# Performance work log

Measured on AMD Instinct MI355X. Metric: run time of the kernel, lower is better.

## Reference

```python
import jax, jax.numpy as jnp
import numpy as np

TWO_PI = 2.0 * np.pi
ALPHA = 0.65
KSIZE = (3, 3, 3)   # (kOr, kH, kW)
ITERS = 1
BN_EPS = 1e-5


def _interp(v, dy, dx):
    """Bilinear sample of v[b,c,o, y+dy[o], x+dx[o]], border-clamped.
    v: [B,C,Or,H,W]; dy, dx: [Or] float per-orientation constant shifts."""
    H, W = v.shape[3], v.shape[4]
    y0 = jnp.floor(dy); fy = dy - y0; y0 = y0.astype(jnp.int32)
    iy = jnp.arange(H)[None, :] + y0[:, None]                      # [Or,H]
    g0 = jnp.take_along_axis(v, jnp.clip(iy, 0, H - 1)[None, None, :, :, None], axis=3)
    g1 = jnp.take_along_axis(v, jnp.clip(iy + 1, 0, H - 1)[None, None, :, :, None], axis=3)
    fyb = fy[None, None, :, None, None]
    v = (1.0 - fyb) * g0 + fyb * g1
    x0 = jnp.floor(dx); fx = dx - x0; x0 = x0.astype(jnp.int32)
    ix = jnp.arange(W)[None, :] + x0[:, None]                      # [Or,W]
    h0 = jnp.take_along_axis(v, jnp.clip(ix, 0, W - 1)[None, None, :, None, :], axis=4)
    h1 = jnp.take_along_axis(v, jnp.clip(ix + 1, 0, W - 1)[None, None, :, None, :], axis=4)
    fxb = fx[None, None, :, None, None]
    return (1.0 - fxb) * h0 + fxb * h1


def _convection(u, g0):
    """out[b,c,p] = u[b,c, p . g0[c]^{-1}] via trilinear resampling.
    Sample point: ((x,y) - R(theta - th0)@(x0,y0), theta - th0), theta periodic."""
    Or = u.shape[2]
    def one(uc, g):  # uc: [B,Or,H,W], g = (x0, y0, th0)
        x0, y0, th0 = g[0], g[1], g[2]
        t = th0 * Or / TWO_PI
        i = jnp.floor(t); f = t - i; i = i.astype(jnp.int32)
        # periodic linear interpolation along orientation axis
        v = (1.0 - f) * jnp.roll(uc, i, axis=1) + f * jnp.roll(uc, i + 1, axis=1)
        a = jnp.arange(Or, dtype=u.dtype) * (TWO_PI / Or) - th0
        dx = -(jnp.cos(a) * x0 - jnp.sin(a) * y0)
        dy = -(jnp.sin(a) * x0 + jnp.cos(a) * y0)
        return _interp(v[:, None], dy, dx)[:, 0]
    return jax.vmap(one, in_axes=(1, 0), out_axes=1)(u, g0)


def _se2_log(qx, qy, dth):
    """Exact SE(2) logarithm coordinates (c1,c2,c3) of group offset (qx,qy,dth)."""
    if abs(dth) < 1e-9:
        return qx, qy, dth
    h = 0.5 * dth
    cot = np.cos(h) / np.sin(h)
    return h * (qx * cot + qy), h * (-qx + qy * cot), dth


def _morph(u, metric, dilate):
    """Fractional morphological dilation (max of u(p.q) - k(q)) or erosion
    (min of u(p.q) + k(q)) with left-invariant Riemannian kernel
    k_c(q) = nu_a * d_c(q)^{2a/(2a-1)}, d_c^2 = (m0*c1)^2+(m1*c2)^2+(m2*c3)^2."""
    kOr, kH, kW = KSIZE
    Or = u.shape[2]
    thetas = jnp.arange(Or, dtype=u.dtype) * (TWO_PI / Or)
    p = 2.0 * ALPHA / (2.0 * ALPHA - 1.0)
    nu = (2.0 * ALPHA - 1.0) * (2.0 * ALPHA) ** (-p)
    out = None
    for qt in range(-(kOr // 2), kOr // 2 + 1):
        dth = qt * TWO_PI / Or
        for qy in range(-(kH // 2), kH // 2 + 1):
            for qx in range(-(kW // 2), kW // 2 + 1):
                c1, c2, c3 = _se2_log(float(qx), float(qy), dth)
                s = (metric[:, 0] * c1) ** 2 + (metric[:, 1] * c2) ** 2 + (metric[:, 2] * c3) ** 2
                k = nu * s ** (p / 2.0)                       # [C]
                # left-invariant shift: spatial offset rotated by theta_o
                dxo = jnp.cos(thetas) * qx - jnp.sin(thetas) * qy
                dyo = jnp.sin(thetas) * qx + jnp.cos(thetas) * qy
                val = _interp(jnp.roll(u, -qt, axis=2), dyo, dxo)
                kb = k[None, :, None, None, None]
                cand = val - kb if dilate else val + kb
                if out is None:
                    out = cand
                else:
                    out = jnp.maximum(out, cand) if dilate else jnp.minimum(out, cand)
    return out


def setup_inputs() -> dict:
    key = jax.random.key(0)
    ks = jax.random.split(key, 5)
    B, Cin, Cout, Or, H, W = 4, 8, 16, 8, 128, 128
    x = jax.random.normal(ks[0], (B, Cin, Or, H, W), dtype=jnp.float32)
    g0 = 0.5 * jax.random.normal(ks[1], (Cin, 3), dtype=jnp.float32)
    lo, hi = 1.4 / 3.0, 0.7 * 3.0   # reset_parameters range for metric params
    metric_dil = jax.random.uniform(ks[2], (Cin, 3), minval=lo, maxval=hi, dtype=jnp.float32)
    metric_ero = jax.random.uniform(ks[3], (Cin, 3), minval=lo, maxval=hi, dtype=jnp.float32)
    bound = 0.25  # kaiming_uniform(a=sqrt(5)) bound for [8,16] weight
    weight = jax.random.uniform(ks[4], (Cin, Cout), minval=-bound, maxval=bound, dtype=jnp.float32)
    gamma = jnp.ones((Cout,), jnp.float32)
    beta = jnp.zeros((Cout,), jnp.float32)
    return dict(x=x, g0=g0, metric_dil=metric_dil, metric_ero=metric_ero,
                weight=weight, gamma=gamma, beta=beta)


def reference(x, g0, metric_dil, metric_ero, weight, gamma, beta):
    u = x
    for _ in range(ITERS):
        u = _convection(u, g0)
        u = _morph(u, metric_dil, dilate=True)
        u = _morph(u, metric_ero, dilate=False)
    # channel mixing: [B,Cin,Or,H,W] x [Cin,Cout] -> [B,Cout,Or,H,W]
    y = jnp.einsum('bcohw,cd->bdohw', u, weight)
    # BatchNorm3d (training mode): per-channel stats over (B,Or,H,W)
    m = y.mean(axis=(0, 2, 3, 4), keepdims=True)
    v = y.var(axis=(0, 2, 3, 4), keepdims=True)
    yh = (y - m) * jax.lax.rsqrt(v + BN_EPS)
    return yh * gamma[None, :, None, None, None] + beta[None, :, None, None, None]
```

## Files before the change

### kernel.cpp

```cpp
#include <hip/hip_runtime.h>
#include <math.h>
#include <utility>

#define B 4
#define CIN 8
#define COUT 16
#define OR_ 8
#define H_ 128
#define W_ 128
#define HW 16384
#define PLANE HW
#define CH_STR (OR_*HW)
#define BATCH_STR (CIN*CH_STR)
#define NELEM (B*BATCH_STR)
#define NPOS (B*OR_*HW)
#define NB_RED 256

#define TILE 16
#define CB_DIM 24
#define CB_S   29
#define CB_PL  (CB_DIM*CB_S)
#define DB_DIM 20
#define DB_S   21
#define DB_PL  (DB_DIM*DB_S)

typedef __attribute__((ext_vector_type(4))) float f4;

struct Tables {
  float kdil[CIN][27];
  float kero[CIN][27];
  int   o1[CIN][OR_], o2[CIN][OR_];
  int   iy0[CIN][OR_], ix0[CIN][OR_];
  float w00[CIN][OR_], w01[CIN][OR_], w10[CIN][OR_], w11[CIN][OR_];
  float cf[CIN];
  int   iymin[CIN], iymax[CIN], ixmin[CIN], ixmax[CIN];
};

__host__ __device__ constexpr double m_cos(int o) {
  const double r = 0.70710678118654752440;
  const double t[8] = {1.0, r, 0.0, -r, -1.0, -r, 0.0, r};
  return t[o];
}
__host__ __device__ constexpr double m_sin(int o) {
  const double r = 0.70710678118654752440;
  const double t[8] = {0.0, r, 1.0, r, 0.0, -r, -1.0, -r};
  return t[o];
}
__host__ __device__ constexpr double tap_dx(int o, int j) {
  return m_cos(o)*(j % 3 - 1) - m_sin(o)*(j / 3 - 1);
}
__host__ __device__ constexpr double tap_dy(int o, int j) {
  return m_sin(o)*(j % 3 - 1) + m_cos(o)*(j / 3 - 1);
}
__host__ __device__ constexpr int ifloor(double v) {
  int i = (int)v;
  return ((double)i > v) ? i - 1 : i;
}
__host__ __device__ constexpr int tap_ix(int o, int j) { return ifloor(tap_dx(o, j)); }
__host__ __device__ constexpr int tap_iy(int o, int j) { return ifloor(tap_dy(o, j)); }
__host__ __device__ constexpr float tap_fx(int o, int j) { return (float)(tap_dx(o, j) - tap_ix(o, j)); }
__host__ __device__ constexpr float tap_fy(int o, int j) { return (float)(tap_dy(o, j) - tap_iy(o, j)); }
__host__ __device__ constexpr float corner_w(int o, int j, int dyb, int dxb) {
  float fy = tap_fy(o, j), fx = tap_fx(o, j);
  return (dyb ? fy : 1.0f - fy) * (dxb ? fx : 1.0f - fx);
}
__host__ __device__ constexpr int corner_r(int o, int j, int dyb) { return tap_iy(o, j) + dyb + 2; }
__host__ __device__ constexpr int corner_c(int o, int j, int i, int dxb) { return i + tap_ix(o, j) + dxb + 2; }
__host__ __device__ constexpr bool row_used(int o, int r) {
  for (int j = 0; j < 9; ++j)
    for (int dyb = 0; dyb < 2; ++dyb)
      for (int dxb = 0; dxb < 2; ++dxb)
        if (corner_w(o, j, dyb, dxb) != 0.0f && corner_r(o, j, dyb) == r)
          return true;
  return false;
}

template<int N> struct Rep {
  template<class F> __device__ __forceinline__ static void run(F&& f) {
    Rep<N-1>::run(f);
    f(std::integral_constant<int, N-1>{});
  }
};
template<> struct Rep<0> {
  template<class F> __device__ __forceinline__ static void run(F&&) {}
};


__global__ void precompute_kernel(const float* __restrict__ g0,
                                  const float* __restrict__ mdil,
                                  const float* __restrict__ mero,
                                  Tables* __restrict__ T) {
  const int t = threadIdx.x;
  const double TWO_PI = 6.283185307179586476925286766559;
  const double P  = 2.0*0.65/(2.0*0.65 - 1.0);
  const double NU = (2.0*0.65 - 1.0)*pow(2.0*0.65, -P);
  if (t < 432) {
    int which = t / 216;
    int r = t % 216;
    int c = r / 27;
    int j = r % 27;
    int qt = j/9 - 1;
    int qy = (j/3)%3 - 1;
    int qx = j%3 - 1;
    double dth = qt * (TWO_PI/OR_);
    double c1, c2, c3;
    if (qt == 0) { c1 = qx; c2 = qy; c3 = 0.0; }
    else {
      double h = 0.5*dth;
      double cot = cos(h)/sin(h);
      c1 = h*(qx*cot + qy);
      c2 = h*(-qx + qy*cot);
      c3 = dth;
    }
    const float* m = which ? mero : mdil;
    double a0 = (double)m[c*3+0]*c1;
    double a1 = (double)m[c*3+1]*c2;
    double a2 = (double)m[c*3+2]*c3;
    double s = a0*a0 + a1*a1 + a2*a2;
    float k = (float)(NU * pow(s, P*0.5));
    if (which) T->kero[c][j] = k; else T->kdil[c][j] = k;
  } else if (t >= 512 && t < 512 + CIN*OR_) {
    int r = t - 512;
    int c = r >> 3;
    int o = r & 7;
    float x0 = g0[c*3+0], y0 = g0[c*3+1], th0 = g0[c*3+2];
    float a = (float)(o*(TWO_PI/OR_)) - th0;
    float ca = cosf(a), sa = sinf(a);
    float dxv = -(ca*x0 - sa*y0);
    float dyv = -(sa*x0 + ca*y0);
    float fy0 = floorf(dyv), fx0 = floorf(dxv);
    float fy = dyv - fy0, fx = dxv - fx0;
    T->iy0[c][o] = (int)fy0;
    T->ix0[c][o] = (int)fx0;
    T->w00[c][o] = (1.f-fy)*(1.f-fx);
    T->w01[c][o] = (1.f-fy)*fx;
    T->w10[c][o] = fy*(1.f-fx);
    T->w11[c][o] = fy*fx;
    float tt = th0 * (float)(OR_/TWO_PI);
    float fi = floorf(tt);
    int ci = (int)fi;
    T->o1[c][o] = (o - ci) & 7;
    T->o2[c][o] = (o - ci - 1) & 7;
    if (o == 0) T->cf[c] = tt - fi;
  }
  __syncthreads();
  if (t < CIN) {
    int iymn = 999, iymx = -999, ixmn = 999, ixmx = -999;
    for (int o = 0; o < OR_; ++o) {
      iymn = min(iymn, T->iy0[t][o]); iymx = max(iymx, T->iy0[t][o]);
      ixmn = min(ixmn, T->ix0[t][o]); ixmx = max(ixmx, T->ix0[t][o]);
    }
    T->iymin[t] = iymn; T->iymax[t] = iymx;
    T->ixmin[t] = ixmn; T->ixmax[t] = ixmx;
  }
}

template<int O, int DIL, int PLSTR, int RSTR>
__device__ __forceinline__ void morph_tile_lds(const float* __restrict__ src,
                                               const float* __restrict__ kt,
                                               int row, int gc, float acc[4]) {
  Rep<3>::run([&](auto qc) {
    constexpr int qti = decltype(qc)::value;
    const float* p = src + ((O + qti + 7) & 7) * PLSTR + row * RSTR + gc;
    float win[5][8];
    Rep<5>::run([&](auto rc) {
      constexpr int r = decltype(rc)::value;
      if constexpr (row_used(O, r)) {
        #pragma unroll
        for (int k = 0; k < 8; ++k) win[r][k] = p[r*RSTR + k];
      }
    });
    Rep<9>::run([&](auto jc) {
      constexpr int j = decltype(jc)::value;
      float k = kt[qti*9 + j];
      float base = DIL ? -k : k;
      Rep<4>::run([&](auto ic) {
        constexpr int i = decltype(ic)::value;
        float v = base;
        Rep<4>::run([&](auto cc2) {
          constexpr int cn  = decltype(cc2)::value;
          constexpr int dyb = cn >> 1, dxb = cn & 1;
          constexpr float Wgt = corner_w(O, j, dyb, dxb);
          if constexpr (Wgt != 0.0f) {
            constexpr int R = corner_r(O, j, dyb);
            constexpr int C = corner_c(O, j, i, dxb);
            v = fmaf(Wgt, win[R][C], v);
          }
        });
        acc[i] = DIL ? fmaxf(acc[i], v) : fminf(acc[i], v);
      });
    });
  });
}

template<int O>
__device__ __forceinline__ void dil_wave(const float* __restrict__ cb, float* __restrict__ db,
                                         const float* __restrict__ kt, int lane) {
  #pragma unroll
  for (int it = 0; it < 2; ++it) {
    int g = lane + it*64;
    if (g < 100) {
      int row = g / 5;
      int gc = (g - row*5) * 4;
      float acc[4] = {-INFINITY, -INFINITY, -INFINITY, -INFINITY};
      morph_tile_lds<O, 1, CB_PL, CB_S>(cb, kt, row, gc, acc);
      float* d = db + O*DB_PL + row*DB_S + gc;
      #pragma unroll
      for (int i = 0; i < 4; ++i) d[i] = acc[i];
    }
  }
}

template<int O>
__device__ __forceinline__ void ero_wave(const float* __restrict__ db, float* __restrict__ dst,
                                         const float* __restrict__ kt, int lane) {
  int row = lane >> 2;
  int gc = (lane & 3) * 4;
  float acc[4] = {INFINITY, INFINITY, INFINITY, INFINITY};
  morph_tile_lds<O, 0, DB_PL, DB_S>(db, kt, row, gc, acc);
  f4 v = {acc[0], acc[1], acc[2], acc[3]};
  *(f4*)(dst + O*PLANE + row*W_ + gc) = v;
}

__global__ __launch_bounds__(512, 4)
void fused_kernel(const float* __restrict__ x, float* __restrict__ u3,
                  const Tables* __restrict__ T) {
  __shared__ float convbuf[8*CB_PL];
  __shared__ float dilbuf[8*DB_PL];
  int blk = blockIdx.x;
  int tx = blk & 7, ty = (blk >> 3) & 7, c = (blk >> 6) & 7, b = blk >> 9;
  int h0 = ty*TILE, w0 = tx*TILE;
  int t = threadIdx.x;
  int wid = t >> 6, lane = t & 63;
  const float* xc = x + b*BATCH_STR + c*CH_STR;

  {
    const int o = wid;
    const int iy0 = T->iy0[c][o], ix0 = T->ix0[c][o];
    const float w00 = T->w00[c][o], w01 = T->w01[c][o];
    const float w10 = T->w10[c][o], w11 = T->w11[c][o];
    const float cfv = T->cf[c];
    const float* p1 = xc + T->o1[c][o]*PLANE;
    const float* p2 = xc + T->o2[c][o]*PLANE;
    bool interior = (h0 - 4 + T->iymin[c] >= 0) & (h0 + 20 + T->iymax[c] <= 127)
                  & (w0 - 4 + T->ixmin[c] >= 0) & (w0 + 20 + T->ixmax[c] <= 127)
                  & (h0 >= 16) & (h0 <= 96) & (w0 >= 16) & (w0 <= 96);
    if (interior) {
      #pragma unroll
      for (int it = 0; it < 3; ++it) {
        int q = lane + it*64;
        if (q < 144) {
          int r = q / 6;
          int cq = q - r*6;
          int iy = h0 - 4 + r + iy0;
          int ix = w0 - 4 + cq*4 + ix0;
          const float* q1 = p1 + iy*W_ + ix;
          const float* q2 = p2 + iy*W_ + ix;
          float a[5], bb[5], cc[5], dd[5];
          #pragma unroll
          for (int k = 0; k < 5; ++k) {
            a[k] = q1[k]; bb[k] = q1[W_+k]; cc[k] = q2[k]; dd[k] = q2[W_+k];
          }
          float* dst = &convbuf[o*CB_PL + r*CB_S + cq*4];
          #pragma unroll
          for (int i = 0; i < 4; ++i) {
            float v1 = w00*a[i] + w01*a[i+1] + w10*bb[i] + w11*bb[i+1];
            float v2 = w00*cc[i] + w01*cc[i+1] + w10*dd[i] + w11*dd[i+1];
            dst[i] = (1.0f - cfv)*v1 + cfv*v2;
          }
        }
      }
    } else {
      #pragma unroll
      for (int it = 0; it < 9; ++it) {
        int cell = lane + it*64;
        int r = cell / 24;
        int col = cell - r*24;
        int gh = min(max(h0 - 4 + r, 0), 127);
        int gw = min(max(w0 - 4 + col, 0), 127);
        int iy = gh + iy0, ix = gw + ix0;
        int r0 = min(max(iy, 0), 127), r1 = min(max(iy+1, 0), 127);
        int c0 = min(max(ix, 0), 127), c1 = min(max(ix+1, 0), 127);
        float v1 = w00*p1[r0*W_+c0] + w01*p1[r0*W_+c1] + w10*p1[r1*W_+c0] + w11*p1[r1*W_+c1];
        float v2 = w00*p2[r0*W_+c0] + w01*p2[r0*W_+c1] + w10*p2[r1*W_+c0] + w11*p2[r1*W_+c1];
        convbuf[o*CB_PL + r*CB_S + col] = (1.0f - cfv)*v1 + cfv*v2;
      }
    }
  }
  __syncthreads();

  {
    const float* kt = T->kdil[c];
    switch (wid) {
      case 0: dil_wave<0>(convbuf, dilbuf, kt, lane); break;
      case 1: dil_wave<1>(convbuf, dilbuf, kt, lane); break;
      case 2: dil_wave<2>(convbuf, dilbuf, kt, lane); break;
      case 3: dil_wave<3>(convbuf, dilbuf, kt, lane); break;
      case 4: dil_wave<4>(convbuf, dilbuf, kt, lane); break;
      case 5: dil_wave<5>(convbuf, dilbuf, kt, lane); break;
      case 6: dil_wave<6>(convbuf, dilbuf, kt, lane); break;
      default: dil_wave<7>(convbuf, dilbuf, kt, lane); break;
    }
  }
  __syncthreads();

  if ((h0 == 0) | (h0 == 112) | (w0 == 0) | (w0 == 112)) {
    #pragma unroll
    for (int k = 0; k < 7; ++k) {
      int cc = t + k*512;
      if (cc < 3200) {
        int col = cc % DB_DIM;
        int tmp = cc / DB_DIM;
        int row = tmp % DB_DIM;
        int o = tmp / DB_DIM;
        int vh = h0 - 2 + row, vw = w0 - 2 + col;
        int dr = min(max(vh, 0), 127) - vh;
        int dc = min(max(vw, 0), 127) - vw;
        if ((dr != 0) | (dc != 0)) {
          dilbuf[o*DB_PL + (row + dr)*DB_S + col + dc] ==
          dilbuf[o*DB_PL + row*DB_S + col];
        }
      }
    }
  }
  __syncthreads();
  if ((h0 == 0) | (h0 == 112) | (w0 == 0) | (w0 == 112)) {
    #pragma unroll
    for (int k = 0; k < 7; ++k) {
      int cc = t + k*512;
      if (cc < 3200) {
        int col = cc % DB_DIM;
        int tmp = cc / DB_DIM;
        int row = tmp % DB_DIM;
        int o = tmp / DB_DIM;
        int vh = h0 - 2 + row, vw = w0 - 2 + col;
        int dr = min(max(vh, 0), 127) - vh;
        int dc = min(max(vw, 0), 127) - vw;
        if ((dr != 0) | (dc != 0)) {
          dilbuf[o*DB_PL + row*DB_S + col] =
            dilbuf[o*DB_PL + (row + dr)*DB_S + col + dc];
        }
      }
    }
  }
  __syncthreads();

  {
    const float* kt = T->kero[c];
    float* dst = u3 + (b*CIN + c)*(OR_*PLANE) + h0*W_ + w0;
    switch (wid) {
      case 0: ero_wave<0>(dilbuf, dst, kt, lane); break;
      case 1: ero_wave<1>(dilbuf, dst, kt, lane); break;
      case 2: ero_wave<2>(dilbuf, dst, kt, lane); break;
      case 3: ero_wave<3>(dilbuf, dst, kt, lane); break;
      case 4: ero_wave<4>(dilbuf, dst, kt, lane); break;
      case 5: ero_wave<5>(dilbuf, dst, kt, lane); break;
      case 6: ero_wave<6>(dilbuf, dst, kt, lane); break;
      default: ero_wave<7>(dilbuf, dst, kt, lane); break;
    }
  }
}

__global__ void gram_kernel(const float* __restrict__ u, double* __restrict__ part) {
  int t8 = blockIdx.x*256 + threadIdx.x;
  int hw = (t8 & 2047) << 3;
  int o  = (t8 >> 11) & 7;
  int b  = t8 >> 14;
  const float* base = u + b*BATCH_STR + o*PLANE + hw;
  f4 v0[8], v1[8];
  #pragma unroll
  for (int c = 0; c < 8; c++) {
    v0[c] = *(const f4*)(base + c*CH_STR);
    v1[c] = *(const f4*)(base + c*CH_STR + 4);
  }
  float S[8], G[36];
  #pragma unroll
  for (int c = 0; c < 8; c++)
    S[c] = (v0[c].x + v0[c].y) + (v0[c].z + v0[c].w)
         + (v1[c].x + v1[c].y) + (v1[c].z + v1[c].w);
  {
    int t = 0;
    #pragma unroll
    for (int c = 0; c < 8; c++)
      #pragma unroll
      for (int c2 = c; c2 < 8; c2++) {
        G[t] = v0[c].x*v0[c2].x + v0[c].y*v0[c2].y + v0[c].z*v0[c2].z + v0[c].w*v0[c2].w
             + v1[c].x*v1[c2].x + v1[c].y*v1[c2].y + v1[c].z*v1[c2].z + v1[c].w*v1[c2].w;
        t++;
      }
  }
  __shared__ double lds[4][44];
  int lane = threadIdx.x & 63;
  int wave = threadIdx.x >> 6;
  for (int t = 0; t < 44; t++) {
    double vv = (double)((t < 8) ? S[t] : G[t-8]);
    for (int off = 32; off; off >>= 1) vv += __shfl_down(vv, off);
    if (lane == 0) lds[wave][t] = vv;
  }
  __syncthreads();
  if (threadIdx.x < 44) {
    part[blockIdx.x*44 + threadIdx.x] =
      lds[0][threadIdx.x] + lds[1][threadIdx.x] + lds[2][threadIdx.x] + lds[3][threadIdx.x];
  }
}

__global__ void stats_kernel(const double* __restrict__ part, const float* __restrict__ weight,
                             const float* __restrict__ gamma, const float* __restrict__ beta,
                             float* __restrict__ ss) {
  __shared__ double tot[44];
  int t = threadIdx.x;
  if (t < 352) {
    int cnt = t >> 3, j = t & 7;
    double s = 0.0;
    #pragma unroll 8
    for (int k = 0; k < 32; ++k) s += part[(j + (k << 3))*44 + cnt];
    s += __shfl_down(s, 4);
    s += __shfl_down(s, 2);
    s += __shfl_down(s, 1);
    if (j == 0) tot[cnt] = s;
  }
  __syncthreads();
  if (t < 16) {
    double m = 0.0;
    for (int c = 0; c < 8; c++) m += (double)weight[c*COUT + t] * tot[c];
    double e2 = 0.0;
    int idx = 8;
    for (int c = 0; c < 8; c++)
      for (int c2 = c; c2 < 8; c2++) {
        double wp = (double)weight[c*COUT + t] * (double)weight[c2*COUT + t];
        e2 += (c2 == c ? 1.0 : 2.0) * wp * tot[idx];
        idx++;
      }
    double N = (double)NPOS;
    m /= N; e2 /= N;
    double var = e2 - m*m;
    double inv = rsqrt(var + 1e-5);
    float sc = (float)(inv * (double)gamma[t]);
    ss[t]      = sc;
    ss[16 + t] = beta[t] - (float)m * sc;
  }
}

__global__ void final_kernel(const float* __restrict__ u, const float* __restrict__ weight,
                             const float* __restrict__ ss, float* __restrict__ out) {
  __shared__ float Wsh[8][16];
  __shared__ float scale[16], shift[16];
  int t = threadIdx.x;
  if (t < 128) Wsh[t >> 4][t & 15] = weight[t];
  if (t < 16) { scale[t] = ss[t]; shift[t] = ss[16 + t]; }
  __syncthreads();
  int t4 = blockIdx.x*256 + threadIdx.x;
  int hw = (t4 & 4095) << 2;
  int o  = (t4 >> 12) & 7;
  int b  = t4 >> 15;
  const float* base = u + b*BATCH_STR + o*PLANE + hw;
  f4 v[8];
  #pragma unroll
  for (int c = 0; c < 8; c++) v[c] = *(const f4*)(base + c*CH_STR);
  float* ob = out + b*(COUT*CH_STR) + o*PLANE + hw;
  #pragma unroll
  for (int d = 0; d < 16; d++) {
    f4 y = {0.f, 0.f, 0.f, 0.f};
    #pragma unroll
    for (int c = 0; c < 8; c++) {
      float wv = Wsh[c][d];
      y.x = fmaf(v[c].x, wv, y.x);
      y.y = fmaf(v[c].y, wv, y.y);
      y.z = fmaf(v[c].z, wv, y.z);
      y.w = fmaf(v[c].w, wv, y.w);
    }
    float sc = scale[d], sh = shift[d];
    f4 r = { fmaf(y.x, sc, sh), fmaf(y.y, sc, sh), fmaf(y.z, sc, sh), fmaf(y.w, sc, sh) };
    *(f4*)(ob + d*CH_STR) = r;
  }
}

extern "C" void kernel_launch(void* const* d_in, const int* in_sizes, int n_in,
                              void* d_out, int out_size, void* d_ws, size_t ws_size,
                              hipStream_t stream) {
  const float* x      = (const float*)d_in[0];
  const float* g0     = (const float*)d_in[1];
  const float* mdil   = (const float*)d_in[2];
  const float* mero   = (const float*)d_in[3];
  const float* weight = (const float*)d_in[4];
  const float* gamma  = (const float*)d_in[5];
  const float* beta   = (const float*)d_in[6];
  float* out = (float*)d_out;

  char* ws = (char*)d_ws;
  Tables* T    = (Tables*)ws;
  float*  ss   = (float*)(ws + 8*1024);
  double* part = (double*)(ws + 16*1024);
  float*  u3   = (float*)(ws + (size_t)1*1024*1024);

  precompute_kernel<<<1, 1024, 0, stream>>>(g0, mdil, mero, T);
  fused_kernel<<<B*CIN*64, 512, 0, stream>>>(x, u3, T);
  gram_kernel<<<NB_RED, 256, 0, stream>>>(u3, part);
  stats_kernel<<<1, 384, 0, stream>>>(part, weight, gamma, beta, ss);
  final_kernel<<<NPOS/4/256, 256, 0, stream>>>(u3, weight, ss, out);
}
```

Before: 116.8 us.

## Use 32x32 tiles with 4x4 register patches and fold table precompute into fused kernel

Tiles grow from 16x16 to 32x32 spatial positions, so the halo overhead per output drops. Each thread now computes a 4x4 output patch from float4 LDS windows, which reuses the loaded window across rows. One shared buffer is reused for the convection and dilation stages. The separate precompute launch is removed: each block computes its channel's kernel weights and interpolation tables in LDS, which cuts one launch at the cost of some redundant transcendental work per block. Risks are higher register pressure (a 16-element accumulator pair plus a window) and fewer blocks (512), which may lower occupancy and load balance.

```diff
diff --git a/kernel.cpp b/kernel.cpp
--- a/kernel.cpp
+++ b/kernel.cpp
@@ -16,25 +16,14 @@
 #define NPOS (B*OR_*HW)
 #define NB_RED 256
 
-#define TILE 16
-#define CB_DIM 24
-#define CB_S   29
-#define CB_PL  (CB_DIM*CB_S)
-#define DB_DIM 20
-#define DB_S   21
-#define DB_PL  (DB_DIM*DB_S)
+#define TILE 32
+#define CBR 40
+#define STR4 11
+#define CB_PL4 (CBR*STR4)
+#define DBR 36
+#define DB_PL4 (DBR*STR4)
 
 typedef __attribute__((ext_vector_type(4))) float f4;
-
-struct Tables {
-  float kdil[CIN][27];
-  float kero[CIN][27];
-  int   o1[CIN][OR_], o2[CIN][OR_];
-  int   iy0[CIN][OR_], ix0[CIN][OR_];
-  float w00[CIN][OR_], w01[CIN][OR_], w10[CIN][OR_], w11[CIN][OR_];
-  float cf[CIN];
-  int   iymin[CIN], iymax[CIN], ixmin[CIN], ixmax[CIN];
-};
 
 __host__ __device__ constexpr double m_cos(int o) {
   const double r = 0.70710678118654752440;
@@ -64,14 +53,19 @@
   float fy = tap_fy(o, j), fx = tap_fx(o, j);
   return (dyb ? fy : 1.0f - fy) * (dxb ? fx : 1.0f - fx);
 }
-__host__ __device__ constexpr int corner_r(int o, int j, int dyb) { return tap_iy(o, j) + dyb + 2; }
-__host__ __device__ constexpr int corner_c(int o, int j, int i, int dxb) { return i + tap_ix(o, j) + dxb + 2; }
-__host__ __device__ constexpr bool row_used(int o, int r) {
+__host__ __device__ constexpr int wrow(int o, int j, int rr, int dyb) {
+  return rr + tap_iy(o, j) + dyb + 2;
+}
+__host__ __device__ constexpr int wcol(int o, int j, int i, int dxb) {
+  return i + tap_ix(o, j) + dxb + 2;
+}
+__host__ __device__ constexpr bool wrow_used(int o, int wr) {
   for (int j = 0; j < 9; ++j)
-    for (int dyb = 0; dyb < 2; ++dyb)
-      for (int dxb = 0; dxb < 2; ++dxb)
-        if (corner_w(o, j, dyb, dxb) != 0.0f && corner_r(o, j, dyb) == r)
-          return true;
+    for (int rr = 0; rr < 4; ++rr)
+      for (int dyb = 0; dyb < 2; ++dyb)
+        for (int dxb = 0; dxb < 2; ++dxb)
+          if (corner_w(o, j, dyb, dxb) != 0.0f && wrow(o, j, rr, dyb) == wr)
+            return true;
   return false;
 }
 
@@ -85,175 +79,164 @@
   template<class F> __device__ __forceinline__ static void run(F&&) {}
 };
 
-
-__global__ void precompute_kernel(const float* __restrict__ g0,
-                                  const float* __restrict__ mdil,
-                                  const float* __restrict__ mero,
-                                  Tables* __restrict__ T) {
-  const int t = threadIdx.x;
-  const double TWO_PI = 6.283185307179586476925286766559;
-  const double P  = 2.0*0.65/(2.0*0.65 - 1.0);
-  const double NU = (2.0*0.65 - 1.0)*pow(2.0*0.65, -P);
-  if (t < 432) {
-    int which = t / 216;
-    int r = t % 216;
-    int c = r / 27;
-    int j = r % 27;
-    int qt = j/9 - 1;
-    int qy = (j/3)%3 - 1;
-    int qx = j%3 - 1;
-    double dth = qt * (TWO_PI/OR_);
-    double c1, c2, c3;
-    if (qt == 0) { c1 = qx; c2 = qy; c3 = 0.0; }
-    else {
-      double h = 0.5*dth;
-      double cot = cos(h)/sin(h);
-      c1 = h*(qx*cot + qy);
-      c2 = h*(-qx + qy*cot);
-      c3 = dth;
-    }
-    const float* m = which ? mero : mdil;
-    double a0 = (double)m[c*3+0]*c1;
-    double a1 = (double)m[c*3+1]*c2;
-    double a2 = (double)m[c*3+2]*c3;
-    double s = a0*a0 + a1*a1 + a2*a2;
-    float k = (float)(NU * pow(s, P*0.5));
-    if (which) T->kero[c][j] = k; else T->kdil[c][j] = k;
-  } else if (t >= 512 && t < 512 + CIN*OR_) {
-    int r = t - 512;
-    int c = r >> 3;
-    int o = r & 7;
-    float x0 = g0[c*3+0], y0 = g0[c*3+1], th0 = g0[c*3+2];
-    float a = (float)(o*(TWO_PI/OR_)) - th0;
-    float ca = cosf(a), sa = sinf(a);
-    float dxv = -(ca*x0 - sa*y0);
-    float dyv = -(sa*x0 + ca*y0);
-    float fy0 = floorf(dyv), fx0 = floorf(dxv);
-    float fy = dyv - fy0, fx = dxv - fx0;
-    T->iy0[c][o] = (int)fy0;
-    T->ix0[c][o] = (int)fx0;
-    T->w00[c][o] = (1.f-fy)*(1.f-fx);
-    T->w01[c][o] = (1.f-fy)*fx;
-    T->w10[c][o] = fy*(1.f-fx);
-    T->w11[c][o] = fy*fx;
-    float tt = th0 * (float)(OR_/TWO_PI);
-    float fi = floorf(tt);
-    int ci = (int)fi;
-    T->o1[c][o] = (o - ci) & 7;
-    T->o2[c][o] = (o - ci - 1) & 7;
-    if (o == 0) T->cf[c] = tt - fi;
-  }
-  __syncthreads();
-  if (t < CIN) {
-    int iymn = 999, iymx = -999, ixmn = 999, ixmx = -999;
-    for (int o = 0; o < OR_; ++o) {
-      iymn = min(iymn, T->iy0[t][o]); iymx = max(iymx, T->iy0[t][o]);
-      ixmn = min(ixmn, T->ix0[t][o]); ixmx = max(ixmx, T->ix0[t][o]);
-    }
-    T->iymin[t] = iymn; T->iymax[t] = iymx;
-    T->ixmin[t] = ixmn; T->ixmax[t] = ixmx;
-  }
-}
-
-template<int O, int DIL, int PLSTR, int RSTR>
-__device__ __forceinline__ void morph_tile_lds(const float* __restrict__ src,
-                                               const float* __restrict__ kt,
-                                               int row, int gc, float acc[4]) {
+template<int O, int DIL, int PLF4>
+__device__ __forceinline__ void morph_patch(const f4* __restrict__ sm,
+                                            const float* __restrict__ kL,
+                                            int rbase, int pcc, float acc[16]) {
   Rep<3>::run([&](auto qc) {
     constexpr int qti = decltype(qc)::value;
-    const float* p = src + ((O + qti + 7) & 7) * PLSTR + row * RSTR + gc;
-    float win[5][8];
-    Rep<5>::run([&](auto rc) {
-      constexpr int r = decltype(rc)::value;
-      if constexpr (row_used(O, r)) {
-        #pragma unroll
-        for (int k = 0; k < 8; ++k) win[r][k] = p[r*RSTR + k];
+    const f4* p = sm + ((O + qti + 7) & 7) * PLF4 + rbase * STR4 + pcc;
+    float kq[9];
+    #pragma unroll
+    for (int jj = 0; jj < 9; ++jj) kq[jj] = kL[qti*9 + jj];
+    f4 wv[8][2];
+    Rep<8>::run([&](auto wrc) {
+      constexpr int wr = decltype(wrc)::value;
+      if constexpr (wrow_used(O, wr)) {
+        wv[wr][0] = p[wr*STR4];
+        wv[wr][1] = p[wr*STR4 + 1];
       }
     });
     Rep<9>::run([&](auto jc) {
       constexpr int j = decltype(jc)::value;
-      float k = kt[qti*9 + j];
-      float base = DIL ? -k : k;
-      Rep<4>::run([&](auto ic) {
-        constexpr int i = decltype(ic)::value;
+      float kk = kq[j];
+      float base = DIL ? -kk : kk;
+      Rep<16>::run([&](auto oc) {
+        constexpr int rr = decltype(oc)::value >> 2;
+        constexpr int i  = decltype(oc)::value & 3;
         float v = base;
         Rep<4>::run([&](auto cc2) {
-          constexpr int cn  = decltype(cc2)::value;
-          constexpr int dyb = cn >> 1, dxb = cn & 1;
+          constexpr int dyb = decltype(cc2)::value >> 1, dxb = decltype(cc2)::value & 1;
           constexpr float Wgt = corner_w(O, j, dyb, dxb);
           if constexpr (Wgt != 0.0f) {
-            constexpr int R = corner_r(O, j, dyb);
-            constexpr int C = corner_c(O, j, i, dxb);
-            v = fmaf(Wgt, win[R][C], v);
+            constexpr int WR = wrow(O, j, rr, dyb);
+            constexpr int WC = wcol(O, j, i, dxb);
+            v = fmaf(Wgt, wv[WR][WC >> 2][WC & 3], v);
           }
         });
-        acc[i] = DIL ? fmaxf(acc[i], v) : fminf(acc[i], v);
+        acc[rr*4+i] = DIL ? fmaxf(acc[rr*4+i], v) : fminf(acc[rr*4+i], v);
       });
     });
   });
 }
 
 template<int O>
-__device__ __forceinline__ void dil_wave(const float* __restrict__ cb, float* __restrict__ db,
-                                         const float* __restrict__ kt, int lane) {
-  #pragma unroll
-  for (int it = 0; it < 2; ++it) {
-    int g = lane + it*64;
-    if (g < 100) {
-      int row = g / 5;
-      int gc = (g - row*5) * 4;
-      float acc[4] = {-INFINITY, -INFINITY, -INFINITY, -INFINITY};
-      morph_tile_lds<O, 1, CB_PL, CB_S>(cb, kt, row, gc, acc);
-      float* d = db + O*DB_PL + row*DB_S + gc;
-      #pragma unroll
-      for (int i = 0; i < 4; ++i) d[i] = acc[i];
-    }
+__device__ __forceinline__ void dil_compute(const f4* __restrict__ sm,
+                                            const float* __restrict__ kL, int lane,
+                                            float accA[16], float accB[16]) {
+  int prA = lane / 9, pcA = lane - prA*9;
+  morph_patch<O, 1, CB_PL4>(sm, kL, prA*4, pcA, accA);
+  int pB = lane + 64;
+  if (pB < 81) {
+    int prB = pB / 9, pcB = pB - prB*9;
+    morph_patch<O, 1, CB_PL4>(sm, kL, prB*4, pcB, accB);
   }
 }
 
 template<int O>
-__device__ __forceinline__ void ero_wave(const float* __restrict__ db, float* __restrict__ dst,
-                                         const float* __restrict__ kt, int lane) {
-  int row = lane >> 2;
-  int gc = (lane & 3) * 4;
-  float acc[4] = {INFINITY, INFINITY, INFINITY, INFINITY};
-  morph_tile_lds<O, 0, DB_PL, DB_S>(db, kt, row, gc, acc);
-  f4 v = {acc[0], acc[1], acc[2], acc[3]};
-  *(f4*)(dst + O*PLANE + row*W_ + gc) = v;
+__device__ __forceinline__ void ero_compute(const f4* __restrict__ sm,
+                                            const float* __restrict__ kL, int lane,
+                                            float* __restrict__ dst) {
+  int pr = lane >> 3, pc = lane & 7;
+  float acc[16];
+  #pragma unroll
+  for (int i = 0; i < 16; ++i) acc[i] = INFINITY;
+  morph_patch<O, 0, DB_PL4>(sm, kL, pr*4, pc, acc);
+  #pragma unroll
+  for (int rr = 0; rr < 4; ++rr) {
+    f4 v = {acc[rr*4+0], acc[rr*4+1], acc[rr*4+2], acc[rr*4+3]};
+    *(f4*)(dst + (pr*4+rr)*W_ + pc*4) = v;
+  }
 }
 
 __global__ __launch_bounds__(512, 4)
-void fused_kernel(const float* __restrict__ x, float* __restrict__ u3,
-                  const Tables* __restrict__ T) {
-  __shared__ float convbuf[8*CB_PL];
-  __shared__ float dilbuf[8*DB_PL];
+void fused_kernel(const float* __restrict__ x,
+                  const float* __restrict__ g0,
+                  const float* __restrict__ mdil,
+                  const float* __restrict__ mero,
+                  float* __restrict__ u3) {
+  __shared__ f4 smem[8*CB_PL4];
+  __shared__ float kdilL[27], keroL[27];
+  __shared__ float cw00[8], cw01[8], cw10[8], cw11[8], ccf[1];
+  __shared__ int   cply1[8], cply2[8], ciy0[8], cix0[8];
+
   int blk = blockIdx.x;
-  int tx = blk & 7, ty = (blk >> 3) & 7, c = (blk >> 6) & 7, b = blk >> 9;
+  int tx = blk & 3, ty = (blk >> 2) & 3, c = (blk >> 4) & 7, b = blk >> 7;
   int h0 = ty*TILE, w0 = tx*TILE;
   int t = threadIdx.x;
   int wid = t >> 6, lane = t & 63;
-  const float* xc = x + b*BATCH_STR + c*CH_STR;
+
+  {
+    const double TWO_PI = 6.283185307179586476925286766559;
+    if (t < 54) {
+      const double P  = 2.0*0.65/(2.0*0.65 - 1.0);
+      const double NU = (2.0*0.65 - 1.0)*pow(2.0*0.65, -P);
+      int which = t / 27;
+      int j = t % 27;
+      int qt = j/9 - 1;
+      int qy = (j/3)%3 - 1;
+      int qx = j%3 - 1;
+      double dth = qt * (TWO_PI/OR_);
+      double c1, c2, c3;
+      if (qt == 0) { c1 = qx; c2 = qy; c3 = 0.0; }
+      else {
+        double h = 0.5*dth;
+        double cot = cos(h)/sin(h);
+        c1 = h*(qx*cot + qy);
+        c2 = h*(-qx + qy*cot);
+        c3 = dth;
+      }
+      const float* m = which ? mero : mdil;
+      double a0 = (double)m[c*3+0]*c1;
+      double a1 = (double)m[c*3+1]*c2;
+      double a2 = (double)m[c*3+2]*c3;
+      double s = a0*a0 + a1*a1 + a2*a2;
+      float k = (float)(NU * pow(s, P*0.5));
+      (which ? keroL : kdilL)[j] = k;
+    } else if (t >= 64 && t < 72) {
+      int o = t - 64;
+      float x0 = g0[c*3+0], y0 = g0[c*3+1], th0 = g0[c*3+2];
+      float a = (float)(o*(TWO_PI/OR_)) - th0;
+      float ca = cosf(a), sa = sinf(a);
+      float dxv = -(ca*x0 - sa*y0);
+      float dyv = -(sa*x0 + ca*y0);
+      float fy0 = floorf(dyv), fx0 = floorf(dxv);
+      float fy = dyv - fy0, fx = dxv - fx0;
+      ciy0[o] = (int)fy0;
+      cix0[o] = (int)fx0;
+      cw00[o] = (1.f-fy)*(1.f-fx);
+      cw01[o] = (1.f-fy)*fx;
+      cw10[o] = fy*(1.f-fx);
+      cw11[o] = fy*fx;
+      float tt = th0 * (float)(OR_/TWO_PI);
+      float fi = floorf(tt);
+      int ci = (int)fi;
+      cply1[o] = (o - ci) & 7;
+      cply2[o] = (o - ci - 1) & 7;
+      if (o == 0) ccf[0] = tt - fi;
+    }
+  }
+  __syncthreads();
 
   {
     const int o = wid;
-    const int iy0 = T->iy0[c][o], ix0 = T->ix0[c][o];
-    const float w00 = T->w00[c][o], w01 = T->w01[c][o];
-    const float w10 = T->w10[c][o], w11 = T->w11[c][o];
-    const float cfv = T->cf[c];
-    const float* p1 = xc + T->o1[c][o]*PLANE;
-    const float* p2 = xc + T->o2[c][o]*PLANE;
-    bool interior = (h0 - 4 + T->iymin[c] >= 0) & (h0 + 20 + T->iymax[c] <= 127)
-                  & (w0 - 4 + T->ixmin[c] >= 0) & (w0 + 20 + T->ixmax[c] <= 127)
-                  & (h0 >= 16) & (h0 <= 96) & (w0 >= 16) & (w0 <= 96);
-    if (interior) {
-      #pragma unroll
-      for (int it = 0; it < 3; ++it) {
-        int q = lane + it*64;
-        if (q < 144) {
-          int r = q / 6;
-          int cq = q - r*6;
-          int iy = h0 - 4 + r + iy0;
-          int ix = w0 - 4 + cq*4 + ix0;
+    const float* p1 = x + b*BATCH_STR + c*CH_STR + cply1[o]*PLANE;
+    const float* p2 = x + b*BATCH_STR + c*CH_STR + cply2[o]*PLANE;
+    const int iy0 = ciy0[o], ix0 = cix0[o];
+    const float w00 = cw00[o], w01 = cw01[o], w10 = cw10[o], w11 = cw11[o];
+    const float cfv = ccf[0];
+    float* cbf = (float*)(smem + o*CB_PL4);
+    #pragma unroll
+    for (int it = 0; it < 7; ++it) {
+      int q = lane + it*64;
+      if (q < 400) {
+        int r = q / 10, cq = q - r*10;
+        int gr = h0 - 4 + r;
+        int gc4 = w0 - 4 + cq*4;
+        int iy = gr + iy0, ix = gc4 + ix0;
+        bool ok = (gr >= 0) & (gr <= 127) & (gc4 >= 0) & (gc4+3 <= 127)
+                & (iy >= 0) & (iy <= 126) & (ix >= 0) & (ix+4 <= 127);
+        if (ok) {
           const float* q1 = p1 + iy*W_ + ix;
           const float* q2 = p2 + iy*W_ + ix;
           float a[5], bb[5], cc[5], dd[5];
@@ -261,102 +244,107 @@
           for (int k = 0; k < 5; ++k) {
             a[k] = q1[k]; bb[k] = q1[W_+k]; cc[k] = q2[k]; dd[k] = q2[W_+k];
           }
-          float* dst = &convbuf[o*CB_PL + r*CB_S + cq*4];
+          f4 res;
           #pragma unroll
           for (int i = 0; i < 4; ++i) {
             float v1 = w00*a[i] + w01*a[i+1] + w10*bb[i] + w11*bb[i+1];
             float v2 = w00*cc[i] + w01*cc[i+1] + w10*dd[i] + w11*dd[i+1];
-            dst[i] = (1.0f - cfv)*v1 + cfv*v2;
+            res[i] = (1.0f - cfv)*v1 + cfv*v2;
+          }
+          *(f4*)(cbf + r*44 + cq*4) = res;
+        } else {
+          int gh = min(max(gr, 0), 127);
+          #pragma unroll
+          for (int i = 0; i < 4; ++i) {
+            int gw = min(max(gc4 + i, 0), 127);
+            int yy = gh + iy0, xx = gw + ix0;
+            int r0 = min(max(yy, 0), 127), r1 = min(max(yy+1, 0), 127);
+            int c0 = min(max(xx, 0), 127), c1 = min(max(xx+1, 0), 127);
+            float v1 = w00*p1[r0*W_+c0] + w01*p1[r0*W_+c1] + w10*p1[r1*W_+c0] + w11*p1[r1*W_+c1];
+            float v2 = w00*p2[r0*W_+c0] + w01*p2[r0*W_+c1] + w10*p2[r1*W_+c0] + w11*p2[r1*W_+c1];
+            cbf[r*44 + cq*4 + i] = (1.0f - cfv)*v1 + cfv*v2;
           }
         }
       }
-    } else {
+    }
+  }
+  __syncthreads();
+
+  float accA[16], accB[16];
+  #pragma unroll
+  for (int i = 0; i < 16; ++i) { accA[i] = -INFINITY; accB[i] = -INFINITY; }
+  switch (wid) {
+    case 0: dil_compute<0>(smem, kdilL, lane, accA, accB); break;
+    case 1: dil_compute<1>(smem, kdilL, lane, accA, accB); break;
+    case 2: dil_compute<2>(smem, kdilL, lane, accA, accB); break;
+    case 3: dil_compute<3>(smem, kdilL, lane, accA, accB); break;
+    case 4: dil_compute<4>(smem, kdilL, lane, accA, accB); break;
+    case 5: dil_compute<5>(smem, kdilL, lane, accA, accB); break;
+    case 6: dil_compute<6>(smem, kdilL, lane, accA, accB); break;
+    default: dil_compute<7>(smem, kdilL, lane, accA, accB); break;
+  }
+  __syncthreads();
+  {
+    f4* db = smem + wid*DB_PL4;
+    int pr = lane / 9, pc = lane - pr*9;
+    f4* d = db + pr*4*STR4 + pc;
+    #pragma unroll
+    for (int rr = 0; rr < 4; ++rr) {
+      f4 v = {accA[rr*4+0], accA[rr*4+1], accA[rr*4+2], accA[rr*4+3]};
+      d[rr*STR4] = v;
+    }
+    if (lane < 17) {
+      int p = lane + 64;
+      int pr2 = p / 9, pc2 = p - pr2*9;
+      f4* d2 = db + pr2*4*STR4 + pc2;
       #pragma unroll
-      for (int it = 0; it < 9; ++it) {
-        int cell = lane + it*64;
-        int r = cell / 24;
-        int col = cell - r*24;
-        int gh = min(max(h0 - 4 + r, 0), 127);
-        int gw = min(max(w0 - 4 + col, 0), 127);
-        int iy = gh + iy0, ix = gw + ix0;
-        int r0 = min(max(iy, 0), 127), r1 = min(max(iy+1, 0), 127);
-        int c0 = min(max(ix, 0), 127), c1 = min(max(ix+1, 0), 127);
-        float v1 = w00*p1[r0*W_+c0] + w01*p1[r0*W_+c1] + w10*p1[r1*W_+c0] + w11*p1[r1*W_+c1];
-        float v2 = w00*p2[r0*W_+c0] + w01*p2[r0*W_+c1] + w10*p2[r1*W_+c0] + w11*p2[r1*W_+c1];
-        convbuf[o*CB_PL + r*CB_S + col] = (1.0f - cfv)*v1 + cfv*v2;
-      }
-    }
-  }
-  __syncthreads();
-
-  {
-    const float* kt = T->kdil[c];
-    switch (wid) {
-      case 0: dil_wave<0>(convbuf, dilbuf, kt, lane); break;
-      case 1: dil_wave<1>(convbuf, dilbuf, kt, lane); break;
-      case 2: dil_wave<2>(convbuf, dilbuf, kt, lane); break;
-      case 3: dil_wave<3>(convbuf, dilbuf, kt, lane); break;
-      case 4: dil_wave<4>(convbuf, dilbuf, kt, lane); break;
-      case 5: dil_wave<5>(convbuf, dilbuf, kt, lane); break;
-      case 6: dil_wave<6>(convbuf, dilbuf, kt, lane); break;
-      default: dil_wave<7>(convbuf, dilbuf, kt, lane); break;
-    }
-  }
-  __syncthreads();
-
-  if ((h0 == 0) | (h0 == 112) | (w0 == 0) | (w0 == 112)) {
-    #pragma unroll
-    for (int k = 0; k < 7; ++k) {
-      int cc = t + k*512;
-      if (cc < 3200) {
-        int col = cc % DB_DIM;
-        int tmp = cc / DB_DIM;
-        int row = tmp % DB_DIM;
-        int o = tmp / DB_DIM;
+      for (int rr = 0; rr < 4; ++rr) {
+        f4 v = {accB[rr*4+0], accB[rr*4+1], accB[rr*4+2], accB[rr*4+3]};
+        d2[rr*STR4] = v;
+      }
+    }
+  }
+  __syncthreads();
+
+  if ((h0 == 0) | (h0 == 96) | (w0 == 0) | (w0 == 96)) {
+    float* df = (float*)smem;
+    #pragma unroll
+    for (int k2 = 0; k2 < 5; ++k2) {
+      int i = t + k2*512;
+      if (i < 2176) {
+        int o = i / 272, rest = i - o*272;
+        int row, col;
+        if (rest < 144) {
+          int rr2 = rest / 36;
+          col = rest - rr2*36;
+          row = (rr2 < 2) ? rr2 : rr2 + 32;
+        } else {
+          int j2 = rest - 144;
+          col = j2 & 3; col = (col < 2) ? col : col + 32;
+          row = 2 + (j2 >> 2);
+        }
         int vh = h0 - 2 + row, vw = w0 - 2 + col;
         int dr = min(max(vh, 0), 127) - vh;
         int dc = min(max(vw, 0), 127) - vw;
-        if ((dr != 0) | (dc != 0)) {
-          dilbuf[o*DB_PL + (row + dr)*DB_S + col + dc] ==
-          dilbuf[o*DB_PL + row*DB_S + col];
+        if ((dr | dc) != 0) {
+          df[(o*DBR + row)*44 + col] = df[(o*DBR + row + dr)*44 + col + dc];
         }
       }
     }
   }
   __syncthreads();
-  if ((h0 == 0) | (h0 == 112) | (w0 == 0) | (w0 == 112)) {
-    #pragma unroll
-    for (int k = 0; k < 7; ++k) {
-      int cc = t + k*512;
-      if (cc < 3200) {
-        int col = cc % DB_DIM;
-        int tmp = cc / DB_DIM;
-        int row = tmp % DB_DIM;
-        int o = tmp / DB_DIM;
-        int vh = h0 - 2 + row, vw = w0 - 2 + col;
-        int dr = min(max(vh, 0), 127) - vh;
-        int dc = min(max(vw, 0), 127) - vw;
-        if ((dr != 0) | (dc != 0)) {
-          dilbuf[o*DB_PL + row*DB_S + col] =
-            dilbuf[o*DB_PL + (row + dr)*DB_S + col + dc];
-        }
-      }
-    }
-  }
-  __syncthreads();
 
   {
-    const float* kt = T->kero[c];
-    float* dst = u3 + (b*CIN + c)*(OR_*PLANE) + h0*W_ + w0;
+    float* dst = u3 + ((b*CIN + c)*OR_ + wid)*PLANE + h0*W_ + w0;
     switch (wid) {
-      case 0: ero_wave<0>(dilbuf, dst, kt, lane); break;
-      case 1: ero_wave<1>(dilbuf, dst, kt, lane); break;
-      case 2: ero_wave<2>(dilbuf, dst, kt, lane); break;
-      case 3: ero_wave<3>(dilbuf, dst, kt, lane); break;
-      case 4: ero_wave<4>(dilbuf, dst, kt, lane); break;
-      case 5: ero_wave<5>(dilbuf, dst, kt, lane); break;
-      case 6: ero_wave<6>(dilbuf, dst, kt, lane); break;
-      default: ero_wave<7>(dilbuf, dst, kt, lane); break;
+      case 0: ero_compute<0>(smem, keroL, lane, dst); break;
+      case 1: ero_compute<1>(smem, keroL, lane, dst); break;
+      case 2: ero_compute<2>(smem, keroL, lane, dst); break;
+      case 3: ero_compute<3>(smem, keroL, lane, dst); break;
+      case 4: ero_compute<4>(smem, keroL, lane, dst); break;
+      case 5: ero_compute<5>(smem, keroL, lane, dst); break;
+      case 6: ero_compute<6>(smem, keroL, lane, dst); break;
+      default: ero_compute<7>(smem, keroL, lane, dst); break;
     }
   }
 }
@@ -488,13 +476,11 @@
   float* out = (float*)d_out;
 
   char* ws = (char*)d_ws;
-  Tables* T    = (Tables*)ws;
   float*  ss   = (float*)(ws + 8*1024);
   double* part = (double*)(ws + 16*1024);
   float*  u3   = (float*)(ws + (size_t)1*1024*1024);
 
-  precompute_kernel<<<1, 1024, 0, stream>>>(g0, mdil, mero, T);
-  fused_kernel<<<B*CIN*64, 512, 0, stream>>>(x, u3, T);
+  fused_kernel<<<B*CIN*16, 512, 0, stream>>>(x, g0, mdil, mero, u3);
   gram_kernel<<<NB_RED, 256, 0, stream>>>(u3, part);
   stats_kernel<<<1, 384, 0, stream>>>(part, weight, gamma, beta, ss);
   final_kernel<<<NPOS/4/256, 256, 0, stream>>>(u3, weight, ss, out);
```

Measured after the change: 155.8 us. +33.5%, slower.
